# Kernel optimization log

Measured on AMD Instinct MI355X. Metric: run time of the kernel, lower is better.

Reference implementation:

```python
import jax, jax.numpy as jnp
import numpy as np

B, C, H, W = 512, 2048, 8, 8   # batch, backbone channels, feature-map HxW (cfg.output_hm_shape)
J = 30                          # smpl.pos_joint_num
CF = 512                        # conv output channels
EPS = 1e-5                      # BatchNorm eps


def setup_inputs() -> dict:
    key = jax.random.key(0)
    ks = jax.random.split(key, 10)
    D = J * (CF + 3)  # 15450
    return {
        "img_feat": jax.random.normal(ks[0], (B, C, H, W), jnp.float32),
        # joint coords in heatmap pixel space [0, W-1] (x, y, z)
        "joint_coord_img": jax.random.uniform(ks[1], (B, J, 3), jnp.float32) * (W - 1),
        "conv_w": jax.random.normal(ks[2], (CF, C), jnp.float32) * 0.02,
        "conv_b": jnp.zeros((CF,), jnp.float32),
        "bn_gamma": jnp.ones((CF,), jnp.float32),
        "bn_beta": jnp.zeros((CF,), jnp.float32),
        "bn_mean": jnp.zeros((CF,), jnp.float32),
        "bn_var": jnp.ones((CF,), jnp.float32),
        "root_w": jax.random.normal(ks[3], (6, D), jnp.float32) * 0.01,
        "root_b": jnp.zeros((6,), jnp.float32),
        "pose_w": jax.random.normal(ks[4], (126, D), jnp.float32) * 0.01,
        "pose_b": jnp.zeros((126,), jnp.float32),
        "shape_w": jax.random.normal(ks[5], (10, C), jnp.float32) * 0.01,
        "shape_b": jnp.zeros((10,), jnp.float32),
        "cam_w": jax.random.normal(ks[6], (3, C), jnp.float32) * 0.01,
        "cam_b": jnp.zeros((3,), jnp.float32),
    }


def _bilinear_sample(feat, xy):
    """Batched bilinear sample == F.grid_sample(align_corners=True, padding='zeros')
    with grid built directly from pixel coords in [0, W-1].
    feat: (B, Cf, H, W), xy: (B, J, 2) pixel coords -> (B, J, Cf)."""
    x, y = xy[..., 0], xy[..., 1]
    x0f, y0f = jnp.floor(x), jnp.floor(y)
    wx1, wy1 = x - x0f, y - y0f
    wx0, wy0 = 1.0 - wx1, 1.0 - wy1
    x0, y0 = x0f.astype(jnp.int32), y0f.astype(jnp.int32)
    x1, y1 = x0 + 1, y0 + 1

    def corner(yi, xi, wt):
        valid = (xi >= 0) & (xi < feat.shape[3]) & (yi >= 0) & (yi < feat.shape[2])
        yc = jnp.clip(yi, 0, feat.shape[2] - 1)
        xc = jnp.clip(xi, 0, feat.shape[3] - 1)
        # gather (B, Cf, J) via vmap over batch
        g = jax.vmap(lambda f, yy, xx: f[:, yy, xx])(feat, yc, xc)
        return g * (wt * valid.astype(feat.dtype))[:, None, :]

    out = (corner(y0, x0, wy0 * wx0) + corner(y0, x1, wy0 * wx1)
           + corner(y1, x0, wy1 * wx0) + corner(y1, x1, wy1 * wx1))
    return jnp.transpose(out, (0, 2, 1))  # (B, J, Cf)


def reference(img_feat, joint_coord_img, conv_w, conv_b, bn_gamma, bn_beta,
              bn_mean, bn_var, root_w, root_b, pose_w, pose_b,
              shape_w, shape_b, cam_w, cam_b):
    bsz = img_feat.shape[0]
    pooled = img_feat.mean(axis=(2, 3))                       # (B, 2048)
    shape_param = pooled @ shape_w.T + shape_b                # (B, 10)
    cam_param = pooled @ cam_w.T + cam_b                      # (B, 3)

    # 1x1 conv + BatchNorm (eval) + ReLU
    f = jnp.einsum('bchw,oc->bohw', img_feat, conv_w) + conv_b[None, :, None, None]
    f = (f - bn_mean[None, :, None, None]) * jax.lax.rsqrt(bn_var + EPS)[None, :, None, None]
    f = jax.nn.relu(f * bn_gamma[None, :, None, None] + bn_beta[None, :, None, None])

    # fused per-joint bilinear gather (replaces the per-joint python loop)
    img_feat_joints = _bilinear_sample(f, joint_coord_img[..., :2])  # (B, J, 512)
    feat = jnp.concatenate([img_feat_joints, joint_coord_img], axis=2)  # (B, J, 515)
    feat = feat.reshape(bsz, -1)                              # (B, 15450)

    root_pose = feat @ root_w.T + root_b                      # (B, 6)
    pose_param = feat @ pose_w.T + pose_b                     # (B, 126)
    return (root_pose, pose_param, shape_param, cam_param)
```

## Files before the change

### kernel.cpp

```cpp
#include <hip/hip_runtime.h>
#include <stdint.h>

typedef __attribute__((ext_vector_type(8))) short bf16x8;
typedef __attribute__((ext_vector_type(4))) float f32x4;

__device__ __forceinline__ unsigned short f2bf(float f) {
    union { float f; uint32_t u; } v; v.f = f;
    uint32_t r = (v.u + 0x7FFFu + ((v.u >> 16) & 1u)) >> 16;
    return (unsigned short)r;
}
__device__ __forceinline__ float bf2f(unsigned short u) {
    union { uint32_t u; float f; } v; v.u = ((uint32_t)u) << 16; return v.f;
}

#define WP_ELEMS  1081344
#define W2P_ELEMS 2211840
#define B_OFF     42240

__global__ void pack_convw_kernel(const float* __restrict__ cw,
                                  const float* __restrict__ sw,
                                  const float* __restrict__ camw,
                                  unsigned short* __restrict__ Wp) {
    int gid = blockIdx.x * 256 + threadIdx.x;
    if (gid >= WP_ELEMS) return;
    int kt  = gid / 16896;
    int rem = gid - kt * 16896;
    int row = rem >> 5;
    int c   = rem & 31;
    int k   = kt * 32 + c;
    float v = 0.f;
    if (row < 512)      v = cw[row * 2048 + k];
    else if (row < 522) v = sw[(row - 512) * 2048 + k];
    else if (row < 525) v = camw[(row - 522) * 2048 + k];
    Wp[gid] = f2bf(v);
}

__global__ void pack_w2_kernel(const float* __restrict__ root_w,
                               const float* __restrict__ pose_w,
                               unsigned short* __restrict__ W2p) {
    int gid = blockIdx.x * 256 + threadIdx.x;
    if (gid >= W2P_ELEMS) return;
    int o2 = gid / 15360;
    int kk = gid - o2 * 15360;
    int j  = kk >> 9;
    int o  = kk & 511;
    int col = j * 515 + o;
    float v = 0.f;
    if (o2 < 6)        v = root_w[o2 * 15450 + col];
    else if (o2 < 132) v = pose_w[(o2 - 6) * 15450 + col];
    W2p[gid] = f2bf(v);
}

__global__ void bn_prep_kernel(const float* cb, const float* g, const float* be,
                               const float* m, const float* v, float* sbws) {
    int o = blockIdx.x * 256 + threadIdx.x;
    if (o >= 512) return;
    float s = g[o] * rsqrtf(v[o] + 1e-5f);
    sbws[2 * o]     = s;
    sbws[2 * o + 1] = be[o] + s * (cb[o] - m[o]);
}

__global__ void init_out_kernel(const float* __restrict__ jc,
                                const float* __restrict__ root_w,
                                const float* __restrict__ pose_w,
                                const float* __restrict__ root_b,
                                const float* __restrict__ pose_b,
                                const float* __restrict__ shape_b,
                                const float* __restrict__ cam_b,
                                float* __restrict__ out) {
    int gid = blockIdx.x * 256 + threadIdx.x;
    if (gid < 67584) {
        int b  = gid / 132;
        int o2 = gid - b * 132;
        const float* wr;
        float acc;
        if (o2 < 6) { wr = root_w + o2 * 15450;       acc = root_b[o2]; }
        else        { wr = pose_w + (o2 - 6) * 15450; acc = pose_b[o2 - 6]; }
        const float* jb = jc + b * 90;
        #pragma unroll
        for (int j = 0; j < 30; ++j) {
            acc += jb[j * 3 + 0] * wr[j * 515 + 512];
            acc += jb[j * 3 + 1] * wr[j * 515 + 513];
            acc += jb[j * 3 + 2] * wr[j * 515 + 514];
        }
        if (o2 < 6) out[b * 6 + o2] = acc;
        else        out[3072 + b * 126 + (o2 - 6)] = acc;
    } else {
        int e = gid - 67584;
        int b = e / 13;
        int s = e - b * 13;
        if (s < 10) out[67584 + b * 10 + s] = shape_b[s];
        else        out[72704 + b * 3 + (s - 10)] = cam_b[s - 10];
    }
}

__global__ __launch_bounds__(256, 2)
void conv_main_kernel(const float* __restrict__ img,
                      const float* __restrict__ jc,
                      const unsigned short* __restrict__ Wp,
                      const float* __restrict__ sbws,
                      unsigned short* __restrict__ sampled,
                      float* __restrict__ out) {
    __shared__ __align__(16) char smem[65536];
    const int t    = threadIdx.x;
    const int lane = t & 63;
    const int w    = t >> 6;
    const int l15  = lane & 15;
    const int quad = lane >> 4;
    const int b    = blockIdx.x;

    f32x4 acc[8][4];
    f32x4 accX;
    #pragma unroll
    for (int mi = 0; mi < 8; ++mi)
        #pragma unroll
        for (int nt = 0; nt < 4; ++nt)
            acc[mi][nt] = (f32x4){0.f, 0.f, 0.f, 0.f};
    accX = (f32x4){0.f, 0.f, 0.f, 0.f};

    const float* gBbase = img + (size_t)b * 131072 + (size_t)(w * 8) * 64 + lane;

    for (int kt = 0; kt < 64; ++kt) {
        __syncthreads();
        const int4* gA = (const int4*)(Wp + (size_t)kt * 16896);
        int4 ta[8];
        #pragma unroll
        for (int i = 0; i < 8; ++i) ta[i] = gA[t + 256 * i];
        int4 ta8;
        if (t < 64) ta8 = gA[t + 2048];
        const float* gB = gBbase + (size_t)(kt * 32) * 64;
        float fb[8];
        #pragma unroll
        for (int j = 0; j < 8; ++j) fb[j] = gB[j * 64];

        #pragma unroll
        for (int i = 0; i < 8; ++i) {
            int c2 = t + 256 * i;
            *(int4*)(smem + (c2 >> 2) * 80 + (c2 & 3) * 16) = ta[i];
        }
        if (t < 64) {
            int c2 = t + 2048;
            *(int4*)(smem + (c2 >> 2) * 80 + (c2 & 3) * 16) = ta8;
        }
        {
            int4 bv;
            bv.x = (int)((uint32_t)f2bf(fb[0]) | ((uint32_t)f2bf(fb[1]) << 16));
            bv.y = (int)((uint32_t)f2bf(fb[2]) | ((uint32_t)f2bf(fb[3]) << 16));
            bv.z = (int)((uint32_t)f2bf(fb[4]) | ((uint32_t)f2bf(fb[5]) << 16));
            bv.w = (int)((uint32_t)f2bf(fb[6]) | ((uint32_t)f2bf(fb[7]) << 16));
            *(int4*)(smem + B_OFF + lane * 80 + w * 16) = bv;
        }
        __syncthreads();

        bf16x8 bfr0 = *(const bf16x8*)(smem + B_OFF + (0  + l15) * 80 + quad * 16);
        bf16x8 bfr1 = *(const bf16x8*)(smem + B_OFF + (16 + l15) * 80 + quad * 16);
        bf16x8 bfr2 = *(const bf16x8*)(smem + B_OFF + (32 + l15) * 80 + quad * 16);
        bf16x8 bfr3 = *(const bf16x8*)(smem + B_OFF + (48 + l15) * 80 + quad * 16);
        #pragma unroll
        for (int mi = 0; mi < 8; ++mi) {
            bf16x8 afr = *(const bf16x8*)(smem + (w * 128 + mi * 16 + l15) * 80 + quad * 16);
            acc[mi][0] = __builtin_amdgcn_mfma_f32_16x16x32_bf16(afr, bfr0, acc[mi][0], 0, 0, 0);
            acc[mi][1] = __builtin_amdgcn_mfma_f32_16x16x32_bf16(afr, bfr1, acc[mi][1], 0, 0, 0);
            acc[mi][2] = __builtin_amdgcn_mfma_f32_16x16x32_bf16(afr, bfr2, acc[mi][2], 0, 0, 0);
            acc[mi][3] = __builtin_amdgcn_mfma_f32_16x16x32_bf16(afr, bfr3, acc[mi][3], 0, 0, 0);
        }
        {
            bf16x8 afrX = *(const bf16x8*)(smem + (512 + l15) * 80 + quad * 16);
            bf16x8 bfrW = *(const bf16x8*)(smem + B_OFF + (w * 16 + l15) * 80 + quad * 16);
            accX = __builtin_amdgcn_mfma_f32_16x16x32_bf16(afrX, bfrW, accX, 0, 0, 0);
        }
    }

    __syncthreads();
    const float2* sb2 = (const float2*)sbws;
    #pragma unroll
    for (int mi = 0; mi < 8; ++mi) {
        #pragma unroll
        for (int r = 0; r < 4; ++r) {
            int row = w * 128 + mi * 16 + quad * 4 + r;
            float2 sb = sb2[row];
            #pragma unroll
            for (int nt = 0; nt < 4; ++nt) {
                int col = nt * 16 + l15;
                float v = fmaxf(acc[mi][nt][r] * sb.x + sb.y, 0.f);
                *(unsigned short*)(smem + row * 128 + (((col + row) & 63) << 1)) = f2bf(v);
            }
        }
    }
    #pragma unroll
    for (int r = 0; r < 4; ++r) {
        float v = accX[r];
        v += __shfl_xor(v, 1);
        v += __shfl_xor(v, 2);
        v += __shfl_xor(v, 4);
        v += __shfl_xor(v, 8);
        if (l15 == 0) {
            int s = quad * 4 + r;
            float val = v * 0.015625f;
            if (s < 10)      atomicAdd(out + 67584 + b * 10 + s, val);
            else if (s < 13) atomicAdd(out + 72704 + b * 3 + (s - 10), val);
        }
    }
    __syncthreads();

    const float* jcb = jc + b * 90;
    unsigned int* outsamp = (unsigned int*)(sampled + (size_t)b * 15360);
    const int o = 2 * t;
    for (int s = 0; s < 30; ++s) {
        float x = jcb[s * 3 + 0];
        float y = jcb[s * 3 + 1];
        float x0f = floorf(x), y0f = floorf(y);
        int x0 = (int)x0f, y0 = (int)y0f;
        int x1 = x0 + 1, y1 = y0 + 1;
        float wx1 = x - x0f, wy1 = y - y0f;
        float wx0 = 1.f - wx1, wy0 = 1.f - wy1;
        float vx0 = (x0 >= 0 && x0 < 8) ? 1.f : 0.f;
        float vx1 = (x1 >= 0 && x1 < 8) ? 1.f : 0.f;
        float vy0 = (y0 >= 0 && y0 < 8) ? 1.f : 0.f;
        float vy1 = (y1 >= 0 && y1 < 8) ? 1.f : 0.f;
        int cx0 = min(max(x0, 0), 7), cx1 = min(max(x1, 0), 7);
        int cy0 = min(max(y0, 0), 7), cy1 = min(max(y1, 0), 7);
        int p00 = cy0 * 8 + cx0, p01 = cy0 * 8 + cx1;
        int p10 = cy1 * 8 + cx0, p11 = cy1 * 8 + cx1;
        float w00 = wy0 * wx0 * vy0 * vx0, w01 = wy0 * wx1 * vy0 * vx1;
        float w10 = wy1 * wx0 * vy1 * vx0, w11 = wy1 * wx1 * vy1 * vx1;
        float vA = w00 * bf2f(*(unsigned short*)(smem + o * 128 + (((p00 + o) & 63) << 1)))
                 + w01 * bf2f(*(unsigned short*)(smem + o * 128 + (((p01 + o) & 63) << 1)))
                 + w10 * bf2f(*(unsigned short*)(smem + o * 128 + (((p10 + o) & 63) << 1)))
                 + w11 * bf2f(*(unsigned short*)(smem + o * 128 + (((p11 + o) & 63) << 1)));
        int o1 = o + 1;
        float vB = w00 * bf2f(*(unsigned short*)(smem + o1 * 128 + (((p00 + o1) & 63) << 1)))
                 + w01 * bf2f(*(unsigned short*)(smem + o1 * 128 + (((p01 + o1) & 63) << 1)))
                 + w10 * bf2f(*(unsigned short*)(smem + o1 * 128 + (((p10 + o1) & 63) << 1)))
                 + w11 * bf2f(*(unsigned short*)(smem + o1 * 128 + (((p11 + o1) & 63) << 1)));
        outsamp[s * 256 + t] = (uint32_t)f2bf(vA) | ((uint32_t)f2bf(vB) << 16);
    }
}

__global__ __launch_bounds__(256, 4)
void gemm2_kernel(const unsigned short* __restrict__ sampled,
                  const unsigned short* __restrict__ W2p,
                  float* __restrict__ out) {
    __shared__ __align__(16) char smem[16640];
    const int t    = threadIdx.x;
    const int lane = t & 63;
    const int w    = t >> 6;
    const int l15  = lane & 15;
    const int quad = lane >> 4;
    const int m0   = blockIdx.x * 64;
    const int j    = blockIdx.y;

    f32x4 acc[9];
    #pragma unroll
    for (int nt = 0; nt < 9; ++nt) acc[nt] = (f32x4){0.f, 0.f, 0.f, 0.f};

    for (int kt = 0; kt < 16; ++kt) {
        __syncthreads();
        {
            int r = t >> 2, ci = t & 3;
            int4 d = *(const int4*)(sampled + (size_t)(m0 + r) * 15360 + j * 512 + kt * 32 + ci * 8);
            *(int4*)(smem + r * 80 + ci * 16) = d;
        }
        #pragma unroll
        for (int i = 0; i < 3; ++i) {
            int c2 = t + 256 * i;
            if (c2 < 576) {
                int r = c2 >> 2, ci = c2 & 3;
                int4 d = *(const int4*)(W2p + (size_t)r * 15360 + j * 512 + kt * 32 + ci * 8);
                *(int4*)(smem + 5120 + r * 80 + ci * 16) = d;
            }
        }
        __syncthreads();
        bf16x8 a = *(const bf16x8*)(smem + (w * 16 + l15) * 80 + quad * 16);
        #pragma unroll
        for (int nt = 0; nt < 9; ++nt) {
            bf16x8 bfv = *(const bf16x8*)(smem + 5120 + (nt * 16 + l15) * 80 + quad * 16);
            acc[nt] = __builtin_amdgcn_mfma_f32_16x16x32_bf16(a, bfv, acc[nt], 0, 0, 0);
        }
    }
    #pragma unroll
    for (int nt = 0; nt < 9; ++nt) {
        int o2 = nt * 16 + l15;
        if (o2 < 132) {
            #pragma unroll
            for (int r = 0; r < 4; ++r) {
                int m = m0 + w * 16 + quad * 4 + r;
                float v = acc[nt][r];
                if (o2 < 6) atomicAdd(out + m * 6 + o2, v);
                else        atomicAdd(out + 3072 + m * 126 + (o2 - 6), v);
            }
        }
    }
}

extern "C" void kernel_launch(void* const* d_in, const int* in_sizes, int n_in,
                              void* d_out, int out_size, void* d_ws, size_t ws_size,
                              hipStream_t stream) {
    const float* img     = (const float*)d_in[0];
    const float* jc      = (const float*)d_in[1];
    const float* conv_w  = (const float*)d_in[2];
    const float* conv_b  = (const float*)d_in[3];
    const float* bn_g    = (const float*)d_in[4];
    const float* bn_be   = (const float*)d_in[5];
    const float* bn_m    = (const float*)d_in[6];
    const float* bn_v    = (const float*)d_in[7];
    const float* root_w  = (const float*)d_in[8];
    const float* root_b  = (const float*)d_in[9];
    const float* pose_w  = (const float*)d_in[10];
    const float* pose_b  = (const float*)d_in[11];
    const float* shape_w = (const float*)d_in[12];
    const float* shape_b = (const float*)d_in[13];
    const float* cam_w   = (const float*)d_in[14];
    const float* cam_b   = (const float*)d_in[15];
    float* out = (float*)d_out;
    char* ws = (char*)d_ws;

    unsigned short* Wp   = (unsigned short*)(ws);
    unsigned short* W2p  = (unsigned short*)(ws + 2162688);
    unsigned short* samp = (unsigned short*)(ws + 2162688 + 4423680);
    float* sbws          = (float*)(ws + 2162688 + 4423680 + 15728640);

    pack_convw_kernel<<<4224, 256, 0, stream>>>(conv_w, shape_w, cam_w, Wp);
    pack_w2_kernel<<<8640, 256, 0, stream>>>(root_w, pose_w, W2p);
    bn_prep_kernel<<<2, 256, 0, stream>>>(conv_b, bn_g, bn_be, bn_m, bn_v, sbws);
    init_out_kernel<<<290, 256, 0, stream>>>(jc, root_w, pose_w, root_b, pose_b,
                                             shape_b, cam_b, out);
    conv_main_kernel<<<512, 256, 0, stream>>>(img, jc, Wp, sbws, samp, out);
    gemm2_kernel<<<dim3(8, 30), 256, 0, stream>>>(samp, W2p, out);
}
```

Baseline: 488.0 us.

## Fold joint coords into GEMM2 K dim and replace atomics with partial-sum reduction

The 90 joint-coordinate columns are appended (in bf16) to the sampled matrix and the packed second-stage weights, so they are handled by an extra 31st K-slice of the MFMA GEMM. This removes the separate init_out kernel. GEMM2 now writes per-slice partial tiles to a workspace buffer, and a new reduce kernel sums them with the biases instead of issuing float atomics. Shape and cam outputs are reduced in shared memory and written directly with their biases. The trade-off is bf16 precision on the joint-coordinate terms, an extra kernel launch, and extra partial-buffer traffic.

```diff
diff --git a/kernel.cpp b/kernel.cpp
--- a/kernel.cpp
+++ b/kernel.cpp
@@ -14,7 +14,8 @@
 }
 
 #define WP_ELEMS  1081344
-#define W2P_ELEMS 2211840
+#define K2        15456
+#define W2P_ELEMS (144 * K2)
 #define B_OFF     42240
 
 __global__ void pack_convw_kernel(const float* __restrict__ cw,
@@ -40,14 +41,23 @@
                                unsigned short* __restrict__ W2p) {
     int gid = blockIdx.x * 256 + threadIdx.x;
     if (gid >= W2P_ELEMS) return;
-    int o2 = gid / 15360;
-    int kk = gid - o2 * 15360;
-    int j  = kk >> 9;
-    int o  = kk & 511;
-    int col = j * 515 + o;
+    int o2 = gid / K2;
+    int kk = gid - o2 * K2;
     float v = 0.f;
-    if (o2 < 6)        v = root_w[o2 * 15450 + col];
-    else if (o2 < 132) v = pose_w[(o2 - 6) * 15450 + col];
+    if (o2 < 132) {
+        const float* wr = (o2 < 6) ? (root_w + o2 * 15450) : (pose_w + (o2 - 6) * 15450);
+        if (kk < 15360) {
+            int j = kk >> 9;
+            int o = kk & 511;
+            v = wr[j * 515 + o];
+        } else {
+            int c = kk - 15360;
+            if (c < 90) {
+                int j = c / 3, d = c - 3 * j;
+                v = wr[j * 515 + 512 + d];
+            }
+        }
+    }
     W2p[gid] = f2bf(v);
 }
 
@@ -60,48 +70,16 @@
     sbws[2 * o + 1] = be[o] + s * (cb[o] - m[o]);
 }
 
-__global__ void init_out_kernel(const float* __restrict__ jc,
-                                const float* __restrict__ root_w,
-                                const float* __restrict__ pose_w,
-                                const float* __restrict__ root_b,
-                                const float* __restrict__ pose_b,
-                                const float* __restrict__ shape_b,
-                                const float* __restrict__ cam_b,
-                                float* __restrict__ out) {
-    int gid = blockIdx.x * 256 + threadIdx.x;
-    if (gid < 67584) {
-        int b  = gid / 132;
-        int o2 = gid - b * 132;
-        const float* wr;
-        float acc;
-        if (o2 < 6) { wr = root_w + o2 * 15450;       acc = root_b[o2]; }
-        else        { wr = pose_w + (o2 - 6) * 15450; acc = pose_b[o2 - 6]; }
-        const float* jb = jc + b * 90;
-        #pragma unroll
-        for (int j = 0; j < 30; ++j) {
-            acc += jb[j * 3 + 0] * wr[j * 515 + 512];
-            acc += jb[j * 3 + 1] * wr[j * 515 + 513];
-            acc += jb[j * 3 + 2] * wr[j * 515 + 514];
-        }
-        if (o2 < 6) out[b * 6 + o2] = acc;
-        else        out[3072 + b * 126 + (o2 - 6)] = acc;
-    } else {
-        int e = gid - 67584;
-        int b = e / 13;
-        int s = e - b * 13;
-        if (s < 10) out[67584 + b * 10 + s] = shape_b[s];
-        else        out[72704 + b * 3 + (s - 10)] = cam_b[s - 10];
-    }
-}
-
 __global__ __launch_bounds__(256, 2)
 void conv_main_kernel(const float* __restrict__ img,
                       const float* __restrict__ jc,
                       const unsigned short* __restrict__ Wp,
                       const float* __restrict__ sbws,
+                      const float* __restrict__ shape_b,
+                      const float* __restrict__ cam_b,
                       unsigned short* __restrict__ sampled,
                       float* __restrict__ out) {
-    __shared__ __align__(16) char smem[65536];
+    __shared__ __align__(16) char smem[65536 + 256];
     const int t    = threadIdx.x;
     const int lane = t & 63;
     const int w    = t >> 6;
@@ -187,6 +165,7 @@
             }
         }
     }
+    float* red = (float*)(smem + 65536);
     #pragma unroll
     for (int r = 0; r < 4; ++r) {
         float v = accX[r];
@@ -194,17 +173,22 @@
         v += __shfl_xor(v, 2);
         v += __shfl_xor(v, 4);
         v += __shfl_xor(v, 8);
-        if (l15 == 0) {
-            int s = quad * 4 + r;
-            float val = v * 0.015625f;
-            if (s < 10)      atomicAdd(out + 67584 + b * 10 + s, val);
-            else if (s < 13) atomicAdd(out + 72704 + b * 3 + (s - 10), val);
-        }
+        if (l15 == 0) red[w * 16 + quad * 4 + r] = v;
     }
     __syncthreads();
 
+    if (t < 16) {
+        float v = (red[t] + red[16 + t] + red[32 + t] + red[48 + t]) * 0.015625f;
+        if (t < 10)      out[67584 + b * 10 + t] = v + shape_b[t];
+        else if (t < 13) out[72704 + b * 3 + (t - 10)] = v + cam_b[t - 10];
+    }
     const float* jcb = jc + b * 90;
-    unsigned int* outsamp = (unsigned int*)(sampled + (size_t)b * 15360);
+    if (t < 96) {
+        float v = (t < 90) ? jcb[t] : 0.f;
+        sampled[(size_t)b * K2 + 15360 + t] = f2bf(v);
+    }
+
+    unsigned int* outsamp = (unsigned int*)(sampled + (size_t)b * K2);
     const int o = 2 * t;
     for (int s = 0; s < 30; ++s) {
         float x = jcb[s * 3 + 0];
@@ -240,7 +224,7 @@
 __global__ __launch_bounds__(256, 4)
 void gemm2_kernel(const unsigned short* __restrict__ sampled,
                   const unsigned short* __restrict__ W2p,
-                  float* __restrict__ out) {
+                  float* __restrict__ part) {
     __shared__ __align__(16) char smem[16640];
     const int t    = threadIdx.x;
     const int lane = t & 63;
@@ -249,16 +233,18 @@
     const int quad = lane >> 4;
     const int m0   = blockIdx.x * 64;
     const int j    = blockIdx.y;
+    const int k0   = j * 512;
+    const int ktn  = (j == 30) ? 3 : 16;
 
     f32x4 acc[9];
     #pragma unroll
     for (int nt = 0; nt < 9; ++nt) acc[nt] = (f32x4){0.f, 0.f, 0.f, 0.f};
 
-    for (int kt = 0; kt < 16; ++kt) {
+    for (int kt = 0; kt < ktn; ++kt) {
         __syncthreads();
         {
             int r = t >> 2, ci = t & 3;
-            int4 d = *(const int4*)(sampled + (size_t)(m0 + r) * 15360 + j * 512 + kt * 32 + ci * 8);
+            int4 d = *(const int4*)(sampled + (size_t)(m0 + r) * K2 + k0 + kt * 32 + ci * 8);
             *(int4*)(smem + r * 80 + ci * 16) = d;
         }
         #pragma unroll
@@ -266,7 +252,7 @@
             int c2 = t + 256 * i;
             if (c2 < 576) {
                 int r = c2 >> 2, ci = c2 & 3;
-                int4 d = *(const int4*)(W2p + (size_t)r * 15360 + j * 512 + kt * 32 + ci * 8);
+                int4 d = *(const int4*)(W2p + (size_t)r * K2 + k0 + kt * 32 + ci * 8);
                 *(int4*)(smem + 5120 + r * 80 + ci * 16) = d;
             }
         }
@@ -278,19 +264,29 @@
             acc[nt] = __builtin_amdgcn_mfma_f32_16x16x32_bf16(a, bfv, acc[nt], 0, 0, 0);
         }
     }
+    float* pout = part + (size_t)(j * 8 + blockIdx.x) * 9216;
     #pragma unroll
     for (int nt = 0; nt < 9; ++nt) {
-        int o2 = nt * 16 + l15;
-        if (o2 < 132) {
-            #pragma unroll
-            for (int r = 0; r < 4; ++r) {
-                int m = m0 + w * 16 + quad * 4 + r;
-                float v = acc[nt][r];
-                if (o2 < 6) atomicAdd(out + m * 6 + o2, v);
-                else        atomicAdd(out + 3072 + m * 126 + (o2 - 6), v);
-            }
-        }
-    }
+        #pragma unroll
+        for (int r = 0; r < 4; ++r) {
+            pout[(w * 16 + quad * 4 + r) * 144 + nt * 16 + l15] = acc[nt][r];
+        }
+    }
+}
+
+__global__ void reduce_out_kernel(const float* __restrict__ part,
+                                  const float* __restrict__ root_b,
+                                  const float* __restrict__ pose_b,
+                                  float* __restrict__ out) {
+    int gid = blockIdx.x * 256 + threadIdx.x;
+    int m  = gid / 132;
+    int o2 = gid - m * 132;
+    float s = (o2 < 6) ? root_b[o2] : pose_b[o2 - 6];
+    const float* p = part + (size_t)(m >> 6) * 9216 + (m & 63) * 144 + o2;
+    #pragma unroll
+    for (int j = 0; j < 31; ++j) s += p[(size_t)j * 8 * 9216];
+    if (o2 < 6) out[m * 6 + o2] = s;
+    else        out[3072 + m * 126 + (o2 - 6)] = s;
 }
 
 extern "C" void kernel_launch(void* const* d_in, const int* in_sizes, int n_in,
@@ -317,14 +313,15 @@
 
     unsigned short* Wp   = (unsigned short*)(ws);
     unsigned short* W2p  = (unsigned short*)(ws + 2162688);
-    unsigned short* samp = (unsigned short*)(ws + 2162688 + 4423680);
-    float* sbws          = (float*)(ws + 2162688 + 4423680 + 15728640);
+    unsigned short* samp = (unsigned short*)(ws + 6614016);
+    float* part          = (float*)(ws + 22440960);
+    float* sbws          = (float*)(ws + 31583232);
 
     pack_convw_kernel<<<4224, 256, 0, stream>>>(conv_w, shape_w, cam_w, Wp);
-    pack_w2_kernel<<<8640, 256, 0, stream>>>(root_w, pose_w, W2p);
+    pack_w2_kernel<<<8694, 256, 0, stream>>>(root_w, pose_w, W2p);
     bn_prep_kernel<<<2, 256, 0, stream>>>(conv_b, bn_g, bn_be, bn_m, bn_v, sbws);
-    init_out_kernel<<<290, 256, 0, stream>>>(jc, root_w, pose_w, root_b, pose_b,
-                                             shape_b, cam_b, out);
-    conv_main_kernel<<<512, 256, 0, stream>>>(img, jc, Wp, sbws, samp, out);
-    gemm2_kernel<<<dim3(8, 30), 256, 0, stream>>>(samp, W2p, out);
-}
+    conv_main_kernel<<<512, 256, 0, stream>>>(img, jc, Wp, sbws, shape_b, cam_b,
+                                              samp, out);
+    gemm2_kernel<<<dim3(8, 31), 256, 0, stream>>>(samp, W2p, part);
+    reduce_out_kernel<<<264, 256, 0, stream>>>(part, root_b, pose_b, out);
+}
```

Result: faster. 473.5 us (-3.0%).
